# Performance work log

Measured on AMD Instinct MI355X. Metric: run time of the kernel, lower is better.

## Reference

```python
import jax, jax.numpy as jnp
import numpy as np

N, E, XD, H, L, G, C = 20000, 320000, 128, 256, 4, 128, 10
EPS = 1e-5


def setup_inputs() -> dict:
    key = jax.random.key(0)
    ks = jax.random.split(key, 24)
    s = 0.05
    inp = {
        "x": jax.random.normal(ks[0], (N, XD), jnp.float32),
        "edge_index": jax.random.randint(ks[1], (2, E), 0, N, jnp.int32),
        "batch": jnp.sort(jax.random.randint(ks[2], (N,), 0, G, jnp.int32)),
        "encW": jax.random.normal(ks[3], (XD, H), jnp.float32) * s,
        "encB": jnp.zeros((H,), jnp.float32),
        "convW": jax.random.normal(ks[4], (L, H, H), jnp.float32) * s,
        "convB": jnp.zeros((L, H), jnp.float32),
        "bnG": jnp.ones((L, H), jnp.float32),
        "bnB": jnp.zeros((L, H), jnp.float32),
        "fcW1": jax.random.normal(ks[5], (H, H), jnp.float32) * s,
        "fcB1": jnp.zeros((H,), jnp.float32),
        "fcG1": jnp.ones((H,), jnp.float32),
        "fcBe1": jnp.zeros((H,), jnp.float32),
        "fcW2": jax.random.normal(ks[6], (H, H), jnp.float32) * s,
        "fcB2": jnp.zeros((H,), jnp.float32),
        "fcG2": jnp.ones((H,), jnp.float32),
        "fcBe2": jnp.zeros((H,), jnp.float32),
        "fcW3": jax.random.normal(ks[7], (H, C), jnp.float32) * s,
        "fcB3": jnp.zeros((C,), jnp.float32),
    }
    return inp


def _bn(h, g, b):
    # BatchNorm1d, training-mode batch statistics (biased var), eps=1e-5
    m = h.mean(0)
    v = h.var(0)
    return g * (h - m) * jax.lax.rsqrt(v + EPS) + b


def _forward(x, edge_index, batch, encW, encB, convW, convB, bnG, bnB,
             fcW1, fcB1, fcG1, fcBe1, fcW2, fcB2, fcG2, fcBe2, fcW3, fcB3):
    src, dst = edge_index[0], edge_index[1]
    # GCN symmetric normalization with implicit self-loops (fill value 1)
    deg = jax.ops.segment_sum(jnp.ones((E,), x.dtype), dst, num_segments=N) + 1.0
    dinv = jax.lax.rsqrt(deg)
    enorm = (dinv[src] * dinv[dst])[:, None]       # [E,1]
    self_norm = (dinv * dinv)[:, None]             # [N,1] self-loop coeff

    h = x @ encW + encB                            # node encoder
    for i in range(L):
        t = h @ convW[i]                           # GCNConv linear (no bias)
        agg = jax.ops.segment_sum(t[src] * enorm, dst, num_segments=N)
        t = agg + t * self_norm + convB[i]         # aggregate + self loop + bias
        h = jax.nn.relu(_bn(t, bnG[i], bnB[i]))    # dropout is identity (eval)

    # global mean pool over graph ids
    sums = jax.ops.segment_sum(h, batch, num_segments=G)
    cnts = jax.ops.segment_sum(jnp.ones((N,), h.dtype), batch, num_segments=G)
    g = sums / jnp.maximum(cnts, 1.0)[:, None]     # [G,H]

    # fc_out: MLP(Linear->BN->ReLU->Linear) -> BN -> Linear
    m = jax.nn.relu(_bn(g @ fcW1 + fcB1, fcG1, fcBe1)) @ fcW2 + fcB2
    m = _bn(m, fcG2, fcBe2)
    return m @ fcW3 + fcB3                         # [G,C]


def reference(x, edge_index, batch, encW, encB, convW, convB, bnG, bnB,
              fcW1, fcB1, fcG1, fcBe1, fcW2, fcB2, fcG2, fcBe2, fcW3, fcB3):
    return _forward(x, edge_index, batch, encW, encB, convW, convB, bnG, bnB,
                    fcW1, fcB1, fcG1, fcBe1, fcW2, fcB2, fcG2, fcBe2, fcW3, fcB3)
```

## Files before the change

kernel.cpp:

```cpp
#include <hip/hip_runtime.h>
#include <hip/hip_bf16.h>
#include <cstddef>

#define N_NODES 20000
#define N_EDGES 320000
#define XDIM 128
#define H 256
#define LAYERS 4
#define G_GRAPHS 128
#define C_OUT 10
#define EPS_BN 1e-5f
#define NSLOT 64

typedef __attribute__((ext_vector_type(8))) short short8;
typedef __attribute__((ext_vector_type(4))) float f32x4;

__global__ void hist_kernel(const int* __restrict__ dst, int* __restrict__ cnt, int E) {
    int e = blockIdx.x * blockDim.x + threadIdx.x;
    if (e < E) atomicAdd(&cnt[dst[e]], 1);
}

__global__ void scan_kernel(const int* __restrict__ cnt, int* __restrict__ rowstart,
                            float* __restrict__ dinv, int N) {
    __shared__ int partial[1024];
    int tid = threadIdx.x;
    int chunk = (N + 1023) / 1024;
    int start = tid * chunk;
    int lsum = 0;
    for (int i = 0; i < chunk; ++i) {
        int idx = start + i;
        if (idx < N) {
            int c = cnt[idx];
            dinv[idx] = 1.0f / sqrtf((float)c + 1.0f);
            lsum += c;
        }
    }
    partial[tid] = lsum;
    __syncthreads();
    for (int off = 1; off < 1024; off <<= 1) {
        int v = (tid >= off) ? partial[tid - off] : 0;
        __syncthreads();
        partial[tid] += v;
        __syncthreads();
    }
    int run = (tid == 0) ? 0 : partial[tid - 1];
    for (int i = 0; i < chunk; ++i) {
        int idx = start + i;
        if (idx < N) { rowstart[idx] = run; run += cnt[idx]; }
    }
    if (tid == 1023) rowstart[N] = partial[1023];
}

__global__ void fill_kernel(const int* __restrict__ src, const int* __restrict__ dst,
                            const int* __restrict__ rowstart, int* __restrict__ cursor,
                            const float* __restrict__ dinv,
                            int* __restrict__ csr_src, float* __restrict__ csr_w, int E) {
    int e = blockIdx.x * blockDim.x + threadIdx.x;
    if (e < E) {
        int s = src[e], d = dst[e];
        int pos = rowstart[d] + atomicAdd(&cursor[d], 1);
        csr_src[pos] = s;
        csr_w[pos] = dinv[s] * dinv[d];
    }
}

__global__ void cast_bf16_kernel(const float* __restrict__ in, __hip_bfloat16* __restrict__ out, int n) {
    int i = blockIdx.x * blockDim.x + threadIdx.x;
    if (i < n) out[i] = __float2bfloat16(in[i]);
}

__global__ void tcast_kernel(const float* __restrict__ in, __hip_bfloat16* __restrict__ out,
                             int R, int C, int layers) {
    int i = blockIdx.x * blockDim.x + threadIdx.x;
    int per = R * C;
    if (i >= per * layers) return;
    int l = i / per, rem = i - l * per;
    int r = rem / C, c = rem - r * C;
    out[(size_t)l * per + (size_t)c * R + r] = __float2bfloat16(in[i]);
}

template <int K>
__global__ __launch_bounds__(256) void gemm_bf16_kernel(
    const __hip_bfloat16* __restrict__ A,
    const __hip_bfloat16* __restrict__ BT,
    const float* __restrict__ bias,
    __hip_bfloat16* __restrict__ Cbf,
    int M, int Nn) {
    __shared__ short As[128 * 32];
    __shared__ short Bs[128 * 32];
    const short* Ash = (const short*)A;
    const short* Bsh = (const short*)BT;
    int tid = threadIdx.x;
    int lane = tid & 63;
    int wave = tid >> 6;
    int quad = lane >> 4;
    int lr = lane & 15;
    int wm = (wave & 1) * 64;
    int wn = (wave >> 1) * 64;
    int Mblk = blockIdx.x * 128;
    int Nblk = blockIdx.y * 128;

    f32x4 acc[4][4];
#pragma unroll
    for (int i = 0; i < 4; ++i)
#pragma unroll
        for (int j = 0; j < 4; ++j) acc[i][j] = (f32x4){0.f, 0.f, 0.f, 0.f};

    for (int k0 = 0; k0 < K; k0 += 32) {
#pragma unroll
        for (int i = 0; i < 2; ++i) {
            int s = i * 256 + tid;
            int row = s >> 2;
            int qs = s & 3;
            int qg = qs ^ ((row >> 1) & 3);
            int arow = Mblk + row; if (arow >= M) arow = M - 1;
            *(float4*)&As[row * 32 + qs * 8] =
                *(const float4*)(Ash + (size_t)arow * K + k0 + qg * 8);
            int brow = Nblk + row;
            *(float4*)&Bs[row * 32 + qs * 8] =
                *(const float4*)(Bsh + (size_t)brow * K + k0 + qg * 8);
        }
        __syncthreads();
        short8 af[4], bfr[4];
#pragma unroll
        for (int mi = 0; mi < 4; ++mi) {
            int r = wm + mi * 16 + lr;
            af[mi] = *(const short8*)&As[r * 32 + (quad ^ ((r >> 1) & 3)) * 8];
        }
#pragma unroll
        for (int ni = 0; ni < 4; ++ni) {
            int r = wn + ni * 16 + lr;
            bfr[ni] = *(const short8*)&Bs[r * 32 + (quad ^ ((r >> 1) & 3)) * 8];
        }
#pragma unroll
        for (int mi = 0; mi < 4; ++mi)
#pragma unroll
            for (int ni = 0; ni < 4; ++ni)
                acc[mi][ni] = __builtin_amdgcn_mfma_f32_16x16x32_bf16(af[mi], bfr[ni], acc[mi][ni], 0, 0, 0);
        __syncthreads();
    }
#pragma unroll
    for (int mi = 0; mi < 4; ++mi) {
#pragma unroll
        for (int r = 0; r < 4; ++r) {
            int m = Mblk + wm + mi * 16 + quad * 4 + r;
            if (m < M) {
#pragma unroll
                for (int ni = 0; ni < 4; ++ni) {
                    int n = Nblk + wn + ni * 16 + lr;
                    float v = acc[mi][ni][r];
                    if (bias) v += bias[n];
                    Cbf[(size_t)m * Nn + n] = __float2bfloat16(v);
                }
            }
        }
    }
}

__global__ __launch_bounds__(256) void agg_kernel(const __hip_bfloat16* __restrict__ t,
                           const int* __restrict__ rowstart,
                           const int* __restrict__ csr_src,
                           const float* __restrict__ csr_w,
                           const float* __restrict__ dinv,
                           const float* __restrict__ convB,
                           float* __restrict__ out,
                           float* __restrict__ spart,
                           int N) {
    __shared__ float4 red[4][64];
    int n = blockIdx.x;
    int wave = threadIdx.x >> 6;
    int lane = threadIdx.x & 63;
    int s = rowstart[n], e = rowstart[n + 1];
    const ushort* tp = (const ushort*)t;
    float a0 = 0.f, a1 = 0.f, a2 = 0.f, a3 = 0.f;
    for (int j0 = s + wave; j0 < e; j0 += 16) {
#pragma unroll
        for (int u = 0; u < 4; ++u) {
            int j = j0 + u * 4;
            int idx = n; float w = 0.f;
            if (j < e) { idx = csr_src[j]; w = csr_w[j]; }
            uint2 v = *(const uint2*)(tp + (size_t)idx * H + lane * 4);
            a0 += __uint_as_float(v.x << 16) * w;
            a1 += __uint_as_float(v.x & 0xffff0000u) * w;
            a2 += __uint_as_float(v.y << 16) * w;
            a3 += __uint_as_float(v.y & 0xffff0000u) * w;
        }
    }
    red[wave][lane] = make_float4(a0, a1, a2, a3);
    __syncthreads();
    int c = threadIdx.x;
    const float* rf = (const float*)red;
    float val = rf[c] + rf[256 + c] + rf[512 + c] + rf[768 + c];
    float dn = dinv[n];
    unsigned sv = tp[(size_t)n * H + c];
    val += __uint_as_float(sv << 16) * (dn * dn) + convB[c];
    out[(size_t)n * H + c] = val;
    float* sp = spart + (size_t)(n & (NSLOT - 1)) * (2 * H);
    atomicAdd(&sp[c], val);
    atomicAdd(&sp[H + c], val * val);
}

__global__ void reduce_stats_kernel(const float* __restrict__ spart, float* __restrict__ stats) {
    int c = blockIdx.x * 256 + threadIdx.x;
    float s = 0.f;
#pragma unroll 8
    for (int i = 0; i < NSLOT; ++i) s += spart[(size_t)i * (2 * H) + c];
    stats[c] = s;
}

__global__ void bnrelu_kernel(const float* __restrict__ t, const float* __restrict__ stats,
                              const float* __restrict__ gamma, const float* __restrict__ beta,
                              __hip_bfloat16* __restrict__ out, int N) {
    int c = threadIdx.x;
    float invN = 1.0f / (float)N;
    float mean = stats[c] * invN;
    float var = stats[H + c] * invN - mean * mean;
    float sc = gamma[c] / sqrtf(var + EPS_BN);
    float sh = beta[c] - mean * sc;
    for (int r = blockIdx.x; r < N; r += gridDim.x) {
        float v = t[(size_t)r * H + c];
        out[(size_t)r * H + c] = __float2bfloat16(fmaxf(v * sc + sh, 0.f));
    }
}

__global__ __launch_bounds__(256) void pool_kernel(const __hip_bfloat16* __restrict__ h,
                            const int* __restrict__ batch,
                            float* __restrict__ g, int N) {
    __shared__ float4 red[4][64];
    int gid = blockIdx.x;
    int lo = 0, hi = N;
    while (lo < hi) { int mid = (lo + hi) >> 1; if (batch[mid] < gid) lo = mid + 1; else hi = mid; }
    int s = lo;
    lo = s; hi = N;
    while (lo < hi) { int mid = (lo + hi) >> 1; if (batch[mid] < gid + 1) lo = mid + 1; else hi = mid; }
    int e = lo;
    int wave = threadIdx.x >> 6;
    int lane = threadIdx.x & 63;
    const ushort* hp = (const ushort*)h;
    float a0 = 0.f, a1 = 0.f, a2 = 0.f, a3 = 0.f;
    for (int r = s + wave; r < e; r += 4) {
        uint2 v = *(const uint2*)(hp + (size_t)r * H + lane * 4);
        a0 += __uint_as_float(v.x << 16);
        a1 += __uint_as_float(v.x & 0xffff0000u);
        a2 += __uint_as_float(v.y << 16);
        a3 += __uint_as_float(v.y & 0xffff0000u);
    }
    red[wave][lane] = make_float4(a0, a1, a2, a3);
    __syncthreads();
    int c = threadIdx.x;
    const float* rf = (const float*)red;
    float sum = rf[c] + rf[256 + c] + rf[512 + c] + rf[768 + c];
    g[(size_t)gid * H + c] = sum / fmaxf((float)(e - s), 1.0f);
}

template <int K, int NN>
__global__ __launch_bounds__(256) void fc_lds_kernel(const float* __restrict__ in,
                                                     const float* __restrict__ W,
                                                     const float* __restrict__ b,
                                                     float* __restrict__ out) {
    __shared__ float row[K];
    int g = blockIdx.x;
    for (int k = threadIdx.x; k < K; k += 256) row[k] = in[(size_t)g * K + k];
    __syncthreads();
    int hc = threadIdx.x;
    if (hc < NN) {
        float acc = b[hc];
#pragma unroll
        for (int k = 0; k < K; ++k) acc += row[k] * W[k * NN + hc];
        out[(size_t)g * NN + hc] = acc;
    }
}

__global__ void fc_out_kernel(const float* __restrict__ in, const float* __restrict__ W,
                              const float* __restrict__ b, float* __restrict__ out) {
    int t = blockIdx.x * blockDim.x + threadIdx.x;
    if (t >= G_GRAPHS * C_OUT) return;
    int g = t / C_OUT, c = t % C_OUT;
    float acc = b[c];
#pragma unroll 16
    for (int k = 0; k < H; ++k) acc += in[(size_t)g * H + k] * W[k * C_OUT + c];
    out[t] = acc;
}

__global__ void bn_head_kernel(const float* __restrict__ in, const float* __restrict__ gamma,
                               const float* __restrict__ beta, float* __restrict__ out,
                               int Grows, int relu) {
    int c = blockIdx.x;
    int r = threadIdx.x;
    __shared__ float red[G_GRAPHS];
    float v = in[r * H + c];
    red[r] = v;
    __syncthreads();
    for (int off = G_GRAPHS / 2; off > 0; off >>= 1) {
        if (r < off) red[r] += red[r + off];
        __syncthreads();
    }
    float mean = red[0] / (float)Grows;
    __syncthreads();
    float d = v - mean;
    red[r] = d * d;
    __syncthreads();
    for (int off = G_GRAPHS / 2; off > 0; off >>= 1) {
        if (r < off) red[r] += red[r + off];
        __syncthreads();
    }
    float var = red[0] / (float)Grows;
    float y = gamma[c] * d / sqrtf(var + EPS_BN) + beta[c];
    if (relu) y = fmaxf(y, 0.f);
    out[r * H + c] = y;
}

extern "C" void kernel_launch(void* const* d_in, const int* in_sizes, int n_in,
                              void* d_out, int out_size, void* d_ws, size_t ws_size,
                              hipStream_t stream) {
    const float* x     = (const float*)d_in[0];
    const int*   edge  = (const int*)d_in[1];
    const int*   batch = (const int*)d_in[2];
    const float* encW  = (const float*)d_in[3];
    const float* encB  = (const float*)d_in[4];
    const float* convW = (const float*)d_in[5];
    const float* convB = (const float*)d_in[6];
    const float* bnG   = (const float*)d_in[7];
    const float* bnB   = (const float*)d_in[8];
    const float* fcW1  = (const float*)d_in[9];
    const float* fcB1  = (const float*)d_in[10];
    const float* fcG1  = (const float*)d_in[11];
    const float* fcBe1 = (const float*)d_in[12];
    const float* fcW2  = (const float*)d_in[13];
    const float* fcB2  = (const float*)d_in[14];
    const float* fcG2  = (const float*)d_in[15];
    const float* fcBe2 = (const float*)d_in[16];
    const float* fcW3  = (const float*)d_in[17];
    const float* fcB3  = (const float*)d_in[18];
    float* out = (float*)d_out;

    const int* srcIdx = edge;
    const int* dstIdx = edge + N_EDGES;

    char* base = (char*)d_ws;
    size_t off = 0;
    auto alloc = [&](size_t bytes) -> void* {
        void* p = base + off;
        off = (off + bytes + 255) & ~(size_t)255;
        return p;
    };
    int*   cnt      = (int*)alloc(N_NODES * 4);
    int*   cursor   = (int*)alloc(N_NODES * 4);
    int*   rowstart = (int*)alloc((N_NODES + 1) * 4);
    float* dinv     = (float*)alloc(N_NODES * 4);
    int*   csr_src  = (int*)alloc(N_EDGES * 4);
    float* csr_w    = (float*)alloc(N_EDGES * 4);
    float* bnstats  = (float*)alloc(LAYERS * 2 * H * 4);
    float* spart    = (float*)alloc((size_t)LAYERS * NSLOT * 2 * H * 4);
    __hip_bfloat16* xbf    = (__hip_bfloat16*)alloc((size_t)N_NODES * XDIM * 2);
    __hip_bfloat16* encWT  = (__hip_bfloat16*)alloc((size_t)H * XDIM * 2);
    __hip_bfloat16* convWT = (__hip_bfloat16*)alloc((size_t)LAYERS * H * H * 2);
    __hip_bfloat16* hbf    = (__hip_bfloat16*)alloc((size_t)N_NODES * H * 2);
    __hip_bfloat16* tbf    = (__hip_bfloat16*)alloc((size_t)N_NODES * H * 2);
    float* t2buf = (float*)alloc((size_t)N_NODES * H * 4);
    float* gpool = (float*)alloc(G_GRAPHS * H * 4);
    float* m1    = (float*)alloc(G_GRAPHS * H * 4);
    float* m2    = (float*)alloc(G_GRAPHS * H * 4);

    hipMemsetAsync(cnt, 0, N_NODES * 4, stream);
    hipMemsetAsync(cursor, 0, N_NODES * 4, stream);
    hipMemsetAsync(spart, 0, (size_t)LAYERS * NSLOT * 2 * H * 4, stream);

    hist_kernel<<<(N_EDGES + 255) / 256, 256, 0, stream>>>(dstIdx, cnt, N_EDGES);
    scan_kernel<<<1, 1024, 0, stream>>>(cnt, rowstart, dinv, N_NODES);
    fill_kernel<<<(N_EDGES + 255) / 256, 256, 0, stream>>>(srcIdx, dstIdx, rowstart, cursor,
                                                           dinv, csr_src, csr_w, N_EDGES);

    cast_bf16_kernel<<<(N_NODES * XDIM + 255) / 256, 256, 0, stream>>>(x, xbf, N_NODES * XDIM);
    tcast_kernel<<<(XDIM * H + 255) / 256, 256, 0, stream>>>(encW, encWT, XDIM, H, 1);
    tcast_kernel<<<(LAYERS * H * H + 255) / 256, 256, 0, stream>>>(convW, convWT, H, H, LAYERS);

    dim3 gridG((N_NODES + 127) / 128, H / 128);
    gemm_bf16_kernel<XDIM><<<gridG, 256, 0, stream>>>(xbf, encWT, encB, hbf, N_NODES, H);

    for (int l = 0; l < LAYERS; ++l) {
        float* spartL = spart + (size_t)l * NSLOT * 2 * H;
        gemm_bf16_kernel<H><<<gridG, 256, 0, stream>>>(hbf, convWT + (size_t)l * H * H, nullptr,
                                                       tbf, N_NODES, H);
        agg_kernel<<<N_NODES, 256, 0, stream>>>(tbf, rowstart, csr_src, csr_w, dinv,
                                                convB + l * H, t2buf, spartL, N_NODES);
        reduce_stats_kernel<<<2, 256, 0, stream>>>(spartL, bnstats + l * 2 * H);
        bnrelu_kernel<<<512, H, 0, stream>>>(t2buf, bnstats + l * 2 * H,
                                             bnG + l * H, bnB + l * H, hbf, N_NODES);
    }

    pool_kernel<<<G_GRAPHS, 256, 0, stream>>>(hbf, batch, gpool, N_NODES);

    fc_lds_kernel<H, H><<<G_GRAPHS, 256, 0, stream>>>(gpool, fcW1, fcB1, m1);
    bn_head_kernel<<<H, G_GRAPHS, 0, stream>>>(m1, fcG1, fcBe1, m1, G_GRAPHS, 1);
    fc_lds_kernel<H, H><<<G_GRAPHS, 256, 0, stream>>>(m1, fcW2, fcB2, m2);
    bn_head_kernel<<<H, G_GRAPHS, 0, stream>>>(m2, fcG2, fcBe2, m2, G_GRAPHS, 0);
    fc_out_kernel<<<(G_GRAPHS * C_OUT + 255) / 256, 256, 0, stream>>>(m2, fcW3, fcB3, out);
}
```

Measured before the change: 538.4 us.

## Use wave-per-node aggregation with register stats and smaller GEMM M-tile

The aggregation kernel changes from one 256-thread block per node, which needed an LDS reduction and per-node atomics, to one wavefront per node. Each wave handles 8 nodes in sequence, walks the edges with 4-way unrolled independent gathers, and keeps BN sum and sum-of-squares in registers, issuing atomics once per wave. This removes the block sync and cuts atomic traffic, but it relies on N being divisible by 4*WPN and adds per-wave imbalance across node degrees. Separately, the GEMM M tile shrinks from 128 to 64 rows, doubling the block count for better CU occupancy at the cost of less B-tile reuse.

```diff
diff --git a/kernel.cpp b/kernel.cpp
--- a/kernel.cpp
+++ b/kernel.cpp
@@ -11,6 +11,7 @@
 #define C_OUT 10
 #define EPS_BN 1e-5f
 #define NSLOT 64
+#define WPN 8
 
 typedef __attribute__((ext_vector_type(8))) short short8;
 typedef __attribute__((ext_vector_type(4))) float f32x4;
@@ -86,7 +87,7 @@
     const float* __restrict__ bias,
     __hip_bfloat16* __restrict__ Cbf,
     int M, int Nn) {
-    __shared__ short As[128 * 32];
+    __shared__ short As[64 * 32];
     __shared__ short Bs[128 * 32];
     const short* Ash = (const short*)A;
     const short* Bsh = (const short*)BT;
@@ -95,35 +96,40 @@
     int wave = tid >> 6;
     int quad = lane >> 4;
     int lr = lane & 15;
-    int wm = (wave & 1) * 64;
+    int wm = (wave & 1) * 32;
     int wn = (wave >> 1) * 64;
-    int Mblk = blockIdx.x * 128;
+    int Mblk = blockIdx.x * 64;
     int Nblk = blockIdx.y * 128;
 
-    f32x4 acc[4][4];
-#pragma unroll
-    for (int i = 0; i < 4; ++i)
+    f32x4 acc[2][4];
+#pragma unroll
+    for (int i = 0; i < 2; ++i)
 #pragma unroll
         for (int j = 0; j < 4; ++j) acc[i][j] = (f32x4){0.f, 0.f, 0.f, 0.f};
 
     for (int k0 = 0; k0 < K; k0 += 32) {
+        {
+            int row = tid >> 2;
+            int qs = tid & 3;
+            int qg = qs ^ ((row >> 1) & 3);
+            int arow = Mblk + row; if (arow >= M) arow = M - 1;
+            *(float4*)&As[row * 32 + qs * 8] =
+                *(const float4*)(Ash + (size_t)arow * K + k0 + qg * 8);
+        }
 #pragma unroll
         for (int i = 0; i < 2; ++i) {
             int s = i * 256 + tid;
             int row = s >> 2;
             int qs = s & 3;
             int qg = qs ^ ((row >> 1) & 3);
-            int arow = Mblk + row; if (arow >= M) arow = M - 1;
-            *(float4*)&As[row * 32 + qs * 8] =
-                *(const float4*)(Ash + (size_t)arow * K + k0 + qg * 8);
             int brow = Nblk + row;
             *(float4*)&Bs[row * 32 + qs * 8] =
                 *(const float4*)(Bsh + (size_t)brow * K + k0 + qg * 8);
         }
         __syncthreads();
-        short8 af[4], bfr[4];
-#pragma unroll
-        for (int mi = 0; mi < 4; ++mi) {
+        short8 af[2], bfr[4];
+#pragma unroll
+        for (int mi = 0; mi < 2; ++mi) {
             int r = wm + mi * 16 + lr;
             af[mi] = *(const short8*)&As[r * 32 + (quad ^ ((r >> 1) & 3)) * 8];
         }
@@ -133,14 +139,14 @@
             bfr[ni] = *(const short8*)&Bs[r * 32 + (quad ^ ((r >> 1) & 3)) * 8];
         }
 #pragma unroll
-        for (int mi = 0; mi < 4; ++mi)
+        for (int mi = 0; mi < 2; ++mi)
 #pragma unroll
             for (int ni = 0; ni < 4; ++ni)
                 acc[mi][ni] = __builtin_amdgcn_mfma_f32_16x16x32_bf16(af[mi], bfr[ni], acc[mi][ni], 0, 0, 0);
         __syncthreads();
     }
 #pragma unroll
-    for (int mi = 0; mi < 4; ++mi) {
+    for (int mi = 0; mi < 2; ++mi) {
 #pragma unroll
         for (int r = 0; r < 4; ++r) {
             int m = Mblk + wm + mi * 16 + quad * 4 + r;
@@ -166,38 +172,76 @@
                            float* __restrict__ out,
                            float* __restrict__ spart,
                            int N) {
-    __shared__ float4 red[4][64];
-    int n = blockIdx.x;
     int wave = threadIdx.x >> 6;
     int lane = threadIdx.x & 63;
-    int s = rowstart[n], e = rowstart[n + 1];
+    int wid = blockIdx.x * 4 + wave;
+    int c0 = lane * 4;
     const ushort* tp = (const ushort*)t;
-    float a0 = 0.f, a1 = 0.f, a2 = 0.f, a3 = 0.f;
-    for (int j0 = s + wave; j0 < e; j0 += 16) {
-#pragma unroll
-        for (int u = 0; u < 4; ++u) {
-            int j = j0 + u * 4;
-            int idx = n; float w = 0.f;
-            if (j < e) { idx = csr_src[j]; w = csr_w[j]; }
-            uint2 v = *(const uint2*)(tp + (size_t)idx * H + lane * 4);
-            a0 += __uint_as_float(v.x << 16) * w;
-            a1 += __uint_as_float(v.x & 0xffff0000u) * w;
-            a2 += __uint_as_float(v.y << 16) * w;
-            a3 += __uint_as_float(v.y & 0xffff0000u) * w;
-        }
-    }
-    red[wave][lane] = make_float4(a0, a1, a2, a3);
-    __syncthreads();
-    int c = threadIdx.x;
-    const float* rf = (const float*)red;
-    float val = rf[c] + rf[256 + c] + rf[512 + c] + rf[768 + c];
-    float dn = dinv[n];
-    unsigned sv = tp[(size_t)n * H + c];
-    val += __uint_as_float(sv << 16) * (dn * dn) + convB[c];
-    out[(size_t)n * H + c] = val;
-    float* sp = spart + (size_t)(n & (NSLOT - 1)) * (2 * H);
-    atomicAdd(&sp[c], val);
-    atomicAdd(&sp[H + c], val * val);
+    float b0 = convB[c0], b1 = convB[c0 + 1], b2 = convB[c0 + 2], b3 = convB[c0 + 3];
+    float sv0 = 0.f, sv1 = 0.f, sv2 = 0.f, sv3 = 0.f;
+    float sq0 = 0.f, sq1 = 0.f, sq2 = 0.f, sq3 = 0.f;
+#pragma unroll 1
+    for (int it = 0; it < WPN; ++it) {
+        int n = wid * WPN + it;
+        int s = rowstart[n], e = rowstart[n + 1];
+        float a0 = 0.f, a1 = 0.f, a2 = 0.f, a3 = 0.f;
+        int j = s;
+        for (; j + 3 < e; j += 4) {
+            int i0 = csr_src[j], i1 = csr_src[j + 1], i2 = csr_src[j + 2], i3 = csr_src[j + 3];
+            float w0 = csr_w[j], w1 = csr_w[j + 1], w2 = csr_w[j + 2], w3 = csr_w[j + 3];
+            uint2 v0 = *(const uint2*)(tp + (size_t)i0 * H + c0);
+            uint2 v1 = *(const uint2*)(tp + (size_t)i1 * H + c0);
+            uint2 v2 = *(const uint2*)(tp + (size_t)i2 * H + c0);
+            uint2 v3 = *(const uint2*)(tp + (size_t)i3 * H + c0);
+            a0 += __uint_as_float(v0.x << 16) * w0;
+            a1 += __uint_as_float(v0.x & 0xffff0000u) * w0;
+            a2 += __uint_as_float(v0.y << 16) * w0;
+            a3 += __uint_as_float(v0.y & 0xffff0000u) * w0;
+            a0 += __uint_as_float(v1.x << 16) * w1;
+            a1 += __uint_as_float(v1.x & 0xffff0000u) * w1;
+            a2 += __uint_as_float(v1.y << 16) * w1;
+            a3 += __uint_as_float(v1.y & 0xffff0000u) * w1;
+            a0 += __uint_as_float(v2.x << 16) * w2;
+            a1 += __uint_as_float(v2.x & 0xffff0000u) * w2;
+            a2 += __uint_as_float(v2.y << 16) * w2;
+            a3 += __uint_as_float(v2.y & 0xffff0000u) * w2;
+            a0 += __uint_as_float(v3.x << 16) * w3;
+            a1 += __uint_as_float(v3.x & 0xffff0000u) * w3;
+            a2 += __uint_as_float(v3.y << 16) * w3;
+            a3 += __uint_as_float(v3.y & 0xffff0000u) * w3;
+        }
+        for (; j < e; ++j) {
+            int i0 = csr_src[j];
+            float w0 = csr_w[j];
+            uint2 v0 = *(const uint2*)(tp + (size_t)i0 * H + c0);
+            a0 += __uint_as_float(v0.x << 16) * w0;
+            a1 += __uint_as_float(v0.x & 0xffff0000u) * w0;
+            a2 += __uint_as_float(v0.y << 16) * w0;
+            a3 += __uint_as_float(v0.y & 0xffff0000u) * w0;
+        }
+        float dn = dinv[n];
+        float ws = dn * dn;
+        uint2 vs = *(const uint2*)(tp + (size_t)n * H + c0);
+        a0 += __uint_as_float(vs.x << 16) * ws + b0;
+        a1 += __uint_as_float(vs.x & 0xffff0000u) * ws + b1;
+        a2 += __uint_as_float(vs.y << 16) * ws + b2;
+        a3 += __uint_as_float(vs.y & 0xffff0000u) * ws + b3;
+        float4 o = make_float4(a0, a1, a2, a3);
+        *(float4*)(out + (size_t)n * H + c0) = o;
+        sv0 += a0; sq0 += a0 * a0;
+        sv1 += a1; sq1 += a1 * a1;
+        sv2 += a2; sq2 += a2 * a2;
+        sv3 += a3; sq3 += a3 * a3;
+    }
+    float* sp = spart + (size_t)(wid & (NSLOT - 1)) * (2 * H);
+    atomicAdd(&sp[c0], sv0);
+    atomicAdd(&sp[c0 + 1], sv1);
+    atomicAdd(&sp[c0 + 2], sv2);
+    atomicAdd(&sp[c0 + 3], sv3);
+    atomicAdd(&sp[H + c0], sq0);
+    atomicAdd(&sp[H + c0 + 1], sq1);
+    atomicAdd(&sp[H + c0 + 2], sq2);
+    atomicAdd(&sp[H + c0 + 3], sq3);
 }
 
 __global__ void reduce_stats_kernel(const float* __restrict__ spart, float* __restrict__ stats) {
@@ -375,15 +419,16 @@
     tcast_kernel<<<(XDIM * H + 255) / 256, 256, 0, stream>>>(encW, encWT, XDIM, H, 1);
     tcast_kernel<<<(LAYERS * H * H + 255) / 256, 256, 0, stream>>>(convW, convWT, H, H, LAYERS);
 
-    dim3 gridG((N_NODES + 127) / 128, H / 128);
+    dim3 gridG((N_NODES + 63) / 64, H / 128);
     gemm_bf16_kernel<XDIM><<<gridG, 256, 0, stream>>>(xbf, encWT, encB, hbf, N_NODES, H);
 
+    int aggBlocks = N_NODES / (4 * WPN);
     for (int l = 0; l < LAYERS; ++l) {
         float* spartL = spart + (size_t)l * NSLOT * 2 * H;
         gemm_bf16_kernel<H><<<gridG, 256, 0, stream>>>(hbf, convWT + (size_t)l * H * H, nullptr,
                                                        tbf, N_NODES, H);
-        agg_kernel<<<N_NODES, 256, 0, stream>>>(tbf, rowstart, csr_src, csr_w, dinv,
-                                                convB + l * H, t2buf, spartL, N_NODES);
+        agg_kernel<<<aggBlocks, 256, 0, stream>>>(tbf, rowstart, csr_src, csr_w, dinv,
+                                                  convB + l * H, t2buf, spartL, N_NODES);
         reduce_stats_kernel<<<2, 256, 0, stream>>>(spartL, bnstats + l * 2 * H);
         bnrelu_kernel<<<512, H, 0, stream>>>(t2buf, bnstats + l * 2 * H,
                                              bnG + l * H, bnB + l * H, hbf, N_NODES);
```

Result: slower. 561.3 us (+4.3%).

## Batch multiple nodes per aggregation block and halve GEMM M tile

Applied to the files above, without the earlier changes.

The aggregation kernel now handles 8 nodes per block. Each half-wave gathers 16-byte rows for one of 8 edge streams, and the per-node BN partial sums stay in registers, so the global atomics are issued once per block instead of once per node. The bf16 GEMM's M tile shrinks from 128 to 64 rows, which doubles the block count for better CU occupancy but gives less reuse per block. Per-node edge loops now run sequentially inside a block with two barriers per node, which may add latency on nodes with few edges.

```diff
diff --git a/kernel.cpp b/kernel.cpp
--- a/kernel.cpp
+++ b/kernel.cpp
@@ -11,6 +11,7 @@
 #define C_OUT 10
 #define EPS_BN 1e-5f
 #define NSLOT 64
+#define NB 8
 
 typedef __attribute__((ext_vector_type(8))) short short8;
 typedef __attribute__((ext_vector_type(4))) float f32x4;
@@ -86,7 +87,7 @@
     const float* __restrict__ bias,
     __hip_bfloat16* __restrict__ Cbf,
     int M, int Nn) {
-    __shared__ short As[128 * 32];
+    __shared__ short As[64 * 32];
     __shared__ short Bs[128 * 32];
     const short* Ash = (const short*)A;
     const short* Bsh = (const short*)BT;
@@ -95,35 +96,40 @@
     int wave = tid >> 6;
     int quad = lane >> 4;
     int lr = lane & 15;
-    int wm = (wave & 1) * 64;
+    int wm = (wave & 1) * 32;
     int wn = (wave >> 1) * 64;
-    int Mblk = blockIdx.x * 128;
+    int Mblk = blockIdx.x * 64;
     int Nblk = blockIdx.y * 128;
 
-    f32x4 acc[4][4];
-#pragma unroll
-    for (int i = 0; i < 4; ++i)
+    f32x4 acc[2][4];
+#pragma unroll
+    for (int i = 0; i < 2; ++i)
 #pragma unroll
         for (int j = 0; j < 4; ++j) acc[i][j] = (f32x4){0.f, 0.f, 0.f, 0.f};
 
     for (int k0 = 0; k0 < K; k0 += 32) {
+        {
+            int row = tid >> 2;
+            int qs = tid & 3;
+            int qg = qs ^ ((row >> 1) & 3);
+            int arow = Mblk + row; if (arow >= M) arow = M - 1;
+            *(float4*)&As[row * 32 + qs * 8] =
+                *(const float4*)(Ash + (size_t)arow * K + k0 + qg * 8);
+        }
 #pragma unroll
         for (int i = 0; i < 2; ++i) {
             int s = i * 256 + tid;
             int row = s >> 2;
             int qs = s & 3;
             int qg = qs ^ ((row >> 1) & 3);
-            int arow = Mblk + row; if (arow >= M) arow = M - 1;
-            *(float4*)&As[row * 32 + qs * 8] =
-                *(const float4*)(Ash + (size_t)arow * K + k0 + qg * 8);
             int brow = Nblk + row;
             *(float4*)&Bs[row * 32 + qs * 8] =
                 *(const float4*)(Bsh + (size_t)brow * K + k0 + qg * 8);
         }
         __syncthreads();
-        short8 af[4], bfr[4];
-#pragma unroll
-        for (int mi = 0; mi < 4; ++mi) {
+        short8 af[2], bfr[4];
+#pragma unroll
+        for (int mi = 0; mi < 2; ++mi) {
             int r = wm + mi * 16 + lr;
             af[mi] = *(const short8*)&As[r * 32 + (quad ^ ((r >> 1) & 3)) * 8];
         }
@@ -133,14 +139,14 @@
             bfr[ni] = *(const short8*)&Bs[r * 32 + (quad ^ ((r >> 1) & 3)) * 8];
         }
 #pragma unroll
-        for (int mi = 0; mi < 4; ++mi)
+        for (int mi = 0; mi < 2; ++mi)
 #pragma unroll
             for (int ni = 0; ni < 4; ++ni)
                 acc[mi][ni] = __builtin_amdgcn_mfma_f32_16x16x32_bf16(af[mi], bfr[ni], acc[mi][ni], 0, 0, 0);
         __syncthreads();
     }
 #pragma unroll
-    for (int mi = 0; mi < 4; ++mi) {
+    for (int mi = 0; mi < 2; ++mi) {
 #pragma unroll
         for (int r = 0; r < 4; ++r) {
             int m = Mblk + wm + mi * 16 + quad * 4 + r;
@@ -166,38 +172,58 @@
                            float* __restrict__ out,
                            float* __restrict__ spart,
                            int N) {
-    __shared__ float4 red[4][64];
-    int n = blockIdx.x;
-    int wave = threadIdx.x >> 6;
-    int lane = threadIdx.x & 63;
-    int s = rowstart[n], e = rowstart[n + 1];
+    __shared__ float red[4][256];
+    int tid = threadIdx.x;
+    int wave = tid >> 6;
+    int lane = tid & 63;
+    int sub = lane >> 5;
+    int hl = lane & 31;
+    int stream = wave * 2 + sub;
+    int c0 = hl * 8;
     const ushort* tp = (const ushort*)t;
-    float a0 = 0.f, a1 = 0.f, a2 = 0.f, a3 = 0.f;
-    for (int j0 = s + wave; j0 < e; j0 += 16) {
-#pragma unroll
-        for (int u = 0; u < 4; ++u) {
-            int j = j0 + u * 4;
-            int idx = n; float w = 0.f;
-            if (j < e) { idx = csr_src[j]; w = csr_w[j]; }
-            uint2 v = *(const uint2*)(tp + (size_t)idx * H + lane * 4);
-            a0 += __uint_as_float(v.x << 16) * w;
-            a1 += __uint_as_float(v.x & 0xffff0000u) * w;
-            a2 += __uint_as_float(v.y << 16) * w;
-            a3 += __uint_as_float(v.y & 0xffff0000u) * w;
-        }
-    }
-    red[wave][lane] = make_float4(a0, a1, a2, a3);
-    __syncthreads();
-    int c = threadIdx.x;
-    const float* rf = (const float*)red;
-    float val = rf[c] + rf[256 + c] + rf[512 + c] + rf[768 + c];
-    float dn = dinv[n];
-    unsigned sv = tp[(size_t)n * H + c];
-    val += __uint_as_float(sv << 16) * (dn * dn) + convB[c];
-    out[(size_t)n * H + c] = val;
-    float* sp = spart + (size_t)(n & (NSLOT - 1)) * (2 * H);
-    atomicAdd(&sp[c], val);
-    atomicAdd(&sp[H + c], val * val);
+    float sv = 0.f, sq = 0.f;
+    int n0 = blockIdx.x * NB;
+#pragma unroll 1
+    for (int it = 0; it < NB; ++it) {
+        int n = n0 + it;
+        int s = rowstart[n], e = rowstart[n + 1];
+        float a[8] = {};
+#pragma unroll 1
+        for (int j0 = s; j0 < e; j0 += 16) {
+#pragma unroll
+            for (int u = 0; u < 2; ++u) {
+                int j = j0 + u * 8 + stream;
+                int idx = n; float w = 0.f;
+                if (j < e) { idx = csr_src[j]; w = csr_w[j]; }
+                uint4 v = *(const uint4*)(tp + (size_t)idx * H + c0);
+                a[0] += __uint_as_float(v.x << 16) * w;
+                a[1] += __uint_as_float(v.x & 0xffff0000u) * w;
+                a[2] += __uint_as_float(v.y << 16) * w;
+                a[3] += __uint_as_float(v.y & 0xffff0000u) * w;
+                a[4] += __uint_as_float(v.z << 16) * w;
+                a[5] += __uint_as_float(v.z & 0xffff0000u) * w;
+                a[6] += __uint_as_float(v.w << 16) * w;
+                a[7] += __uint_as_float(v.w & 0xffff0000u) * w;
+            }
+        }
+#pragma unroll
+        for (int k = 0; k < 8; ++k) a[k] += __shfl_xor(a[k], 32);
+        if (sub == 0) {
+            *(float4*)&red[wave][c0] = make_float4(a[0], a[1], a[2], a[3]);
+            *(float4*)&red[wave][c0 + 4] = make_float4(a[4], a[5], a[6], a[7]);
+        }
+        __syncthreads();
+        int c = tid;
+        float val = red[0][c] + red[1][c] + red[2][c] + red[3][c];
+        float dn = dinv[n];
+        val += __bfloat162float(t[(size_t)n * H + c]) * (dn * dn) + convB[c];
+        out[(size_t)n * H + c] = val;
+        sv += val; sq += val * val;
+        __syncthreads();
+    }
+    float* sp = spart + (size_t)(blockIdx.x & (NSLOT - 1)) * (2 * H);
+    atomicAdd(&sp[tid], sv);
+    atomicAdd(&sp[H + tid], sq);
 }
 
 __global__ void reduce_stats_kernel(const float* __restrict__ spart, float* __restrict__ stats) {
@@ -375,15 +401,15 @@
     tcast_kernel<<<(XDIM * H + 255) / 256, 256, 0, stream>>>(encW, encWT, XDIM, H, 1);
     tcast_kernel<<<(LAYERS * H * H + 255) / 256, 256, 0, stream>>>(convW, convWT, H, H, LAYERS);
 
-    dim3 gridG((N_NODES + 127) / 128, H / 128);
+    dim3 gridG((N_NODES + 63) / 64, H / 128);
     gemm_bf16_kernel<XDIM><<<gridG, 256, 0, stream>>>(xbf, encWT, encB, hbf, N_NODES, H);
 
     for (int l = 0; l < LAYERS; ++l) {
         float* spartL = spart + (size_t)l * NSLOT * 2 * H;
         gemm_bf16_kernel<H><<<gridG, 256, 0, stream>>>(hbf, convWT + (size_t)l * H * H, nullptr,
                                                        tbf, N_NODES, H);
-        agg_kernel<<<N_NODES, 256, 0, stream>>>(tbf, rowstart, csr_src, csr_w, dinv,
-                                                convB + l * H, t2buf, spartL, N_NODES);
+        agg_kernel<<<N_NODES / NB, 256, 0, stream>>>(tbf, rowstart, csr_src, csr_w, dinv,
+                                                     convB + l * H, t2buf, spartL, N_NODES);
         reduce_stats_kernel<<<2, 256, 0, stream>>>(spartL, bnstats + l * 2 * H);
         bnrelu_kernel<<<512, H, 0, stream>>>(t2buf, bnstats + l * 2 * H,
                                              bnG + l * H, bnB + l * H, hbf, N_NODES);
```

Measured after the change: 493.9 us. 8.3% less time.
